# Kernel tuning notes

Hardware: AMD Instinct MI355X
Metric: run time of the kernel (lower is better)

## Reference

```python
import jax, jax.numpy as jnp
import numpy as np

N, D = 262144, 64
L, K = 4, 1024


def setup_inputs() -> dict:
    key = jax.random.key(0)
    k1, k2 = jax.random.split(key)
    features = jax.random.normal(k1, (N, D), dtype=jnp.float32)
    codebooks = jax.random.normal(k2, (L, K, D), dtype=jnp.float32)
    return {"features": features, "codebooks": codebooks}


def reference(features, codebooks):
    """Residual VQ: per level, nearest-center (L2) argmin, gather, subtract.

    Uses squared distances (same argmin as torch.cdist p=2).
    """

    def step(residuals, centers):
        # ||r - c||^2 = ||r||^2 - 2 r.c + ||c||^2   -> [N, K]
        d = (
            jnp.sum(residuals * residuals, axis=1, keepdims=True)
            - 2.0 * (residuals @ centers.T)
            + jnp.sum(centers * centers, axis=1)
        )
        idx = jnp.argmin(d, axis=1)          # [N] int32
        quantized = centers[idx]             # [N, D] gather
        return residuals - quantized, (quantized, idx)

    _, (quantized_levels, indices) = jax.lax.scan(step, features, codebooks)
    quantized_result = jnp.sum(quantized_levels, axis=0)  # sum over L levels
    return quantized_result, indices  # indices: [L, N]
```

## Files before the change

### kernel.cpp

```cpp
#include <hip/hip_runtime.h>
#include <math.h>

constexpr int RVQ_N = 262144;
constexpr int RVQ_D = 64;
constexpr int RVQ_L = 4;
constexpr int RVQ_K = 1024;

typedef __attribute__((ext_vector_type(8))) short short8;
typedef __attribute__((ext_vector_type(4))) float floatx4;

__device__ __forceinline__ unsigned short f2bf(float f) {
  unsigned int u = __float_as_uint(f);
  u += 0x7fffu + ((u >> 16) & 1u);
  return (unsigned short)(u >> 16);
}
__device__ __forceinline__ float bf2f(unsigned short h) {
  return __uint_as_float(((unsigned int)h) << 16);
}
__device__ __forceinline__ void split2(float x, unsigned short& h0,
                                       unsigned short& h1) {
  h0 = f2bf(x);
  float r1 = x - bf2f(h0);
  h1 = f2bf(r1);
}

__global__ __launch_bounds__(256) void rvq_prep_split(
    const float* __restrict__ cb, unsigned short* __restrict__ bh,
    unsigned short* __restrict__ bm) {
  int i = blockIdx.x * 256 + threadIdx.x;
  float c2 = -2.0f * cb[i];
  unsigned short h0, h1;
  split2(c2, h0, h1);
  bh[i] = h0;
  bm[i] = h1;
}

__global__ __launch_bounds__(256) void rvq_cnorm_kernel(
    const float* __restrict__ cb, float* __restrict__ cnorm) {
  int i = blockIdx.x * blockDim.x + threadIdx.x;
  const float* c = cb + (size_t)i * RVQ_D;
  float a0 = 0.f, a1 = 0.f, a2 = 0.f, a3 = 0.f;
#pragma unroll
  for (int d = 0; d < RVQ_D; d += 4) {
    float4 v = *reinterpret_cast<const float4*>(c + d);
    a0 = fmaf(v.x, v.x, a0);
    a1 = fmaf(v.y, v.y, a1);
    a2 = fmaf(v.z, v.z, a2);
    a3 = fmaf(v.w, v.w, a3);
  }
  cnorm[i] = (a0 + a1) + (a2 + a3);
}

__device__ __forceinline__ int raddr(int wbase, int p, int d) {
  return d * 256 + wbase + ((p + d) & 63);
}

__device__ __forceinline__ void merge16(float& a1, int& ai1, float& a2,
                                        int& ai2) {
#pragma unroll
  for (int off = 1; off <= 8; off <<= 1) {
    float ob1 = __shfl_xor(a1, off);
    int oi1 = __shfl_xor(ai1, off);
    float ob2 = __shfl_xor(a2, off);
    int oi2 = __shfl_xor(ai2, off);
    bool aw = (a1 < ob1) || (a1 == ob1 && ai1 <= oi1);
    float w1 = aw ? a1 : ob1;
    int wi1 = aw ? ai1 : oi1;
    float l1 = aw ? ob1 : a1;
    int li1 = aw ? oi1 : ai1;
    float w2 = aw ? a2 : ob2;
    int wi2 = aw ? ai2 : oi2;
    bool sw = (l1 < w2) || (l1 == w2 && li1 < wi2);
    a1 = w1;
    ai1 = wi1;
    a2 = sw ? l1 : w2;
    ai2 = sw ? li1 : wi2;
  }
}

__device__ __forceinline__ void load_bt(const unsigned short* __restrict__ bh,
                                        const unsigned short* __restrict__ bmp,
                                        const float* __restrict__ cnl, int nt,
                                        int m, int q, short8 (&b)[2][2],
                                        float& cc) {
  size_t rowoff = (size_t)(nt * 16 + m) * RVQ_D + q * 8;
  b[0][0] = *(const short8*)(bh + rowoff);
  b[0][1] = *(const short8*)(bh + rowoff + 32);
  b[1][0] = *(const short8*)(bmp + rowoff);
  b[1][1] = *(const short8*)(bmp + rowoff + 32);
  cc = cnl[nt * 16 + m];
}

__global__ __launch_bounds__(256, 2) void rvq_mfma_kernel(
    const float* __restrict__ feat, const float* __restrict__ cb,
    const unsigned short* __restrict__ cb_hi,
    const unsigned short* __restrict__ cb_mid,
    const float* __restrict__ cnorm, float* __restrict__ out_q,
    float* __restrict__ out_idx) {
  __shared__ float rlds[RVQ_D * 256];

  const int tid = threadIdx.x;
  const int lane = tid & 63;
  const int wave = tid >> 6;
  const int wbase = wave * 64;
  const int m = lane & 15;
  const int q = lane >> 4;
  const int g = blockIdx.x * 256 + tid;

  {
    const float4* f4 = (const float4*)(feat + (size_t)g * RVQ_D);
#pragma unroll
    for (int i = 0; i < 16; ++i) {
      float4 v = f4[i];
      rlds[raddr(wbase, lane, 4 * i + 0)] = v.x;
      rlds[raddr(wbase, lane, 4 * i + 1)] = v.y;
      rlds[raddr(wbase, lane, 4 * i + 2)] = v.z;
      rlds[raddr(wbase, lane, 4 * i + 3)] = v.w;
    }
  }
  __syncthreads();

  constexpr int AC[3] = {0, 0, 1};
  constexpr int BC[3] = {0, 1, 0};

  for (int l = 0; l < RVQ_L; ++l) {
    const unsigned short* bh = cb_hi + (size_t)l * RVQ_K * RVQ_D;
    const unsigned short* bmp = cb_mid + (size_t)l * RVQ_K * RVQ_D;
    const float* cnl = cnorm + (size_t)l * RVQ_K;
    const float* cbl = cb + (size_t)l * RVQ_K * RVQ_D;

    short8 afr[4][2][2];
#pragma unroll
    for (int t = 0; t < 4; ++t)
#pragma unroll
      for (int oct = 0; oct < 2; ++oct)
#pragma unroll
        for (int j = 0; j < 8; ++j) {
          int d = oct * 32 + q * 8 + j;
          float x = rlds[raddr(wbase, t * 16 + m, d)];
          unsigned short h0, h1;
          split2(x, h0, h1);
          afr[t][0][oct][j] = (short)h0;
          afr[t][1][oct][j] = (short)h1;
        }

    float m1[4][4], m2v[4][4];
    int i1[4][4], i2v[4][4];
#pragma unroll
    for (int t = 0; t < 4; ++t)
#pragma unroll
      for (int r2 = 0; r2 < 4; ++r2) {
        m1[t][r2] = INFINITY;
        m2v[t][r2] = INFINITY;
        i1[t][r2] = 0;
        i2v[t][r2] = 0;
      }

    short8 bA[2][2], bB[2][2];
    float ccA, ccB;
    load_bt(bh, bmp, cnl, 0, m, q, bA, ccA);

    for (int nt = 0; nt < RVQ_K / 16; nt += 2) {
      load_bt(bh, bmp, cnl, nt + 1, m, q, bB, ccB);

      {
        floatx4 acc[4];
#pragma unroll
        for (int t = 0; t < 4; ++t) {
          acc[t][0] = ccA;
          acc[t][1] = ccA;
          acc[t][2] = ccA;
          acc[t][3] = ccA;
        }
#pragma unroll
        for (int s = 0; s < 3; ++s)
#pragma unroll
          for (int oct = 0; oct < 2; ++oct)
#pragma unroll
            for (int t = 0; t < 4; ++t)
              acc[t] = __builtin_amdgcn_mfma_f32_16x16x32_bf16(
                  afr[t][AC[s]][oct], bA[BC[s]][oct], acc[t], 0, 0, 0);
        int kidx = nt * 16 + m;
#pragma unroll
        for (int t = 0; t < 4; ++t)
#pragma unroll
          for (int r2 = 0; r2 < 4; ++r2) {
            float sc = acc[t][r2];
            float om1 = m1[t][r2];
            bool b1 = sc < om1;
            bool b2 = sc < m2v[t][r2];
            m1[t][r2] = fminf(sc, om1);
            m2v[t][r2] = fminf(fmaxf(sc, om1), m2v[t][r2]);
            i2v[t][r2] = b1 ? i1[t][r2] : (b2 ? kidx : i2v[t][r2]);
            i1[t][r2] = b1 ? kidx : i1[t][r2];
          }
      }

      int ntn = (nt + 2 < RVQ_K / 16) ? nt + 2 : nt;
      load_bt(bh, bmp, cnl, ntn, m, q, bA, ccA);

      {
        floatx4 acc[4];
#pragma unroll
        for (int t = 0; t < 4; ++t) {
          acc[t][0] = ccB;
          acc[t][1] = ccB;
          acc[t][2] = ccB;
          acc[t][3] = ccB;
        }
#pragma unroll
        for (int s = 0; s < 3; ++s)
#pragma unroll
          for (int oct = 0; oct < 2; ++oct)
#pragma unroll
            for (int t = 0; t < 4; ++t)
              acc[t] = __builtin_amdgcn_mfma_f32_16x16x32_bf16(
                  afr[t][AC[s]][oct], bB[BC[s]][oct], acc[t], 0, 0, 0);
        int kidx = (nt + 1) * 16 + m;
#pragma unroll
        for (int t = 0; t < 4; ++t)
#pragma unroll
          for (int r2 = 0; r2 < 4; ++r2) {
            float sc = acc[t][r2];
            float om1 = m1[t][r2];
            bool b1 = sc < om1;
            bool b2 = sc < m2v[t][r2];
            m1[t][r2] = fminf(sc, om1);
            m2v[t][r2] = fminf(fmaxf(sc, om1), m2v[t][r2]);
            i2v[t][r2] = b1 ? i1[t][r2] : (b2 ? kidx : i2v[t][r2]);
            i1[t][r2] = b1 ? kidx : i1[t][r2];
          }
      }
    }

    int cand[4] = {0, 0, 0, 0};
    const int srcl = ((lane >> 2) & 3) << 4;
#pragma unroll
    for (int t = 0; t < 4; ++t)
#pragma unroll
      for (int r2 = 0; r2 < 4; ++r2) {
        float p1 = m1[t][r2], p2 = m2v[t][r2];
        int gi1 = i1[t][r2], gi2 = i2v[t][r2];
        merge16(p1, gi1, p2, gi2);
        float x1 = m1[t][r2], x2 = m2v[t][r2];
        int y1 = i1[t][r2], y2 = i2v[t][r2];
        if (y1 == gi1 || y1 == gi2) x1 = INFINITY;
        if (y2 == gi1 || y2 == gi2) x2 = INFINITY;
        if (x2 < x1 || (x2 == x1 && y2 < y1)) {
          float tf = x1; x1 = x2; x2 = tf;
          int ti = y1; y1 = y2; y2 = ti;
        }
        merge16(x1, y1, x2, y2);
        int v1 = __shfl(gi1, srcl);
        int v2 = __shfl(gi2, srcl);
        int v3 = __shfl(y1, srcl);
        int v4 = __shfl(y2, srcl);
        bool take = (q == t) && ((lane & 3) == r2);
        cand[0] = take ? v1 : cand[0];
        cand[1] = take ? v2 : cand[1];
        cand[2] = take ? v3 : cand[2];
        cand[3] = take ? v4 : cand[3];
      }

    {
      int tmp;
      if (cand[0] > cand[1]) { tmp = cand[0]; cand[0] = cand[1]; cand[1] = tmp; }
      if (cand[2] > cand[3]) { tmp = cand[2]; cand[2] = cand[3]; cand[3] = tmp; }
      if (cand[0] > cand[2]) { tmp = cand[0]; cand[0] = cand[2]; cand[2] = tmp; }
      if (cand[1] > cand[3]) { tmp = cand[1]; cand[1] = cand[3]; cand[3] = tmp; }
      if (cand[1] > cand[2]) { tmp = cand[1]; cand[1] = cand[2]; cand[2] = tmp; }
    }

    float r_[RVQ_D];
#pragma unroll
    for (int d = 0; d < RVQ_D; ++d) r_[d] = rlds[raddr(wbase, lane, d)];

    float s0 = 0.f, s1 = 0.f, s2 = 0.f, s3 = 0.f;
#pragma unroll
    for (int i = 0; i < 16; ++i) {
      s0 = fmaf(r_[4 * i + 0], r_[4 * i + 0], s0);
      s1 = fmaf(r_[4 * i + 1], r_[4 * i + 1], s1);
      s2 = fmaf(r_[4 * i + 2], r_[4 * i + 2], s2);
      s3 = fmaf(r_[4 * i + 3], r_[4 * i + 3], s3);
    }
    const float rr = (s0 + s1) + (s2 + s3);

    float best = INFINITY;
    int ci = 0;
#pragma unroll
    for (int jc = 0; jc < 4; ++jc) {
      int k = cand[jc];
      const float4* c4 = (const float4*)(cbl + (size_t)k * RVQ_D);
      float a0 = 0.f, a1 = 0.f, a2 = 0.f, a3 = 0.f;
#pragma unroll
      for (int i = 0; i < 16; ++i) {
        float4 v = c4[i];
        a0 = fmaf(r_[4 * i + 0], v.x, a0);
        a1 = fmaf(r_[4 * i + 1], v.y, a1);
        a2 = fmaf(r_[4 * i + 2], v.z, a2);
        a3 = fmaf(r_[4 * i + 3], v.w, a3);
      }
      float dot = (a0 + a1) + (a2 + a3);
      float score = (rr - 2.0f * dot) + cnl[k];
      if (score < best) {
        best = score;
        ci = k;
      }
    }

    const float4* crow = (const float4*)(cbl + (size_t)ci * RVQ_D);
    if (l < RVQ_L - 1) {
#pragma unroll
      for (int i = 0; i < 16; ++i) {
        float4 v = crow[i];
        rlds[raddr(wbase, lane, 4 * i + 0)] = r_[4 * i + 0] - v.x;
        rlds[raddr(wbase, lane, 4 * i + 1)] = r_[4 * i + 1] - v.y;
        rlds[raddr(wbase, lane, 4 * i + 2)] = r_[4 * i + 2] - v.z;
        rlds[raddr(wbase, lane, 4 * i + 3)] = r_[4 * i + 3] - v.w;
      }
    } else {
      const float4* f4 = (const float4*)(feat + (size_t)g * RVQ_D);
      float4* o4 = (float4*)(out_q + (size_t)g * RVQ_D);
#pragma unroll
      for (int i = 0; i < 16; ++i) {
        float4 v = crow[i];
        float4 f = f4[i];
        float rn0 = r_[4 * i + 0] - v.x;
        float rn1 = r_[4 * i + 1] - v.y;
        float rn2 = r_[4 * i + 2] - v.z;
        float rn3 = r_[4 * i + 3] - v.w;
        float4 o;
        o.x = f.x - rn0;
        o.y = f.y - rn1;
        o.z = f.z - rn2;
        o.w = f.w - rn3;
        o4[i] = o;
      }
    }
    out_idx[(size_t)l * RVQ_N + g] = (float)ci;
    __syncthreads();
  }
}

extern "C" void kernel_launch(void* const* d_in, const int* in_sizes, int n_in,
                              void* d_out, int out_size, void* d_ws,
                              size_t ws_size, hipStream_t stream) {
  const float* features = (const float*)d_in[0];
  const float* codebooks = (const float*)d_in[1];
  float* out_q = (float*)d_out;
  float* out_idx = (float*)d_out + (size_t)RVQ_N * RVQ_D;

  const size_t comp_elems = (size_t)RVQ_L * RVQ_K * RVQ_D;
  unsigned short* cb_hi = (unsigned short*)d_ws;
  unsigned short* cb_mid = cb_hi + comp_elems;
  float* cnorm = (float*)(cb_mid + comp_elems);

  hipLaunchKernelGGL(rvq_prep_split, dim3(comp_elems / 256), dim3(256), 0,
                     stream, codebooks, cb_hi, cb_mid);
  hipLaunchKernelGGL(rvq_cnorm_kernel, dim3((RVQ_L * RVQ_K) / 256), dim3(256),
                     0, stream, codebooks, cnorm);
  hipLaunchKernelGGL(rvq_mfma_kernel, dim3(RVQ_N / 256), dim3(256), 0, stream,
                     features, codebooks, cb_hi, cb_mid, cnorm, out_q,
                     out_idx);
}
```

Before: 1.102 ms.

## Pack score and tile index into sortable uint keys, drop LDS residual buffer

Distance scores are offset by a constant (cnorm+256) so they stay positive, then their low mantissa bits are replaced by the tile index. Top-2 tracking becomes plain unsigned min/max, and the cross-lane merge becomes four shuffle-min passes. The shared-memory residual buffer and its block barriers are removed: residuals are rebuilt each level from features minus the previously chosen codewords, read from global memory, and occupancy is raised to 3 blocks. The risks are extra global/cache traffic for rebuilding residuals, and loss of score precision in the truncated bits, which the exact fp32 rescoring of 4 candidates must absorb.

```diff
diff --git a/kernel.cpp b/kernel.cpp
--- a/kernel.cpp
+++ b/kernel.cpp
@@ -22,6 +22,12 @@
   h0 = f2bf(x);
   float r1 = x - bf2f(h0);
   h1 = f2bf(r1);
+}
+__device__ __forceinline__ void load8(const float* p, float* v) {
+  float4 a = *(const float4*)p;
+  float4 b = *(const float4*)(p + 4);
+  v[0] = a.x; v[1] = a.y; v[2] = a.z; v[3] = a.w;
+  v[4] = b.x; v[5] = b.y; v[6] = b.z; v[7] = b.w;
 }
 
 __global__ __launch_bounds__(256) void rvq_prep_split(
@@ -36,7 +42,8 @@
 }
 
 __global__ __launch_bounds__(256) void rvq_cnorm_kernel(
-    const float* __restrict__ cb, float* __restrict__ cnorm) {
+    const float* __restrict__ cb, float* __restrict__ cnorm,
+    float* __restrict__ cnormB) {
   int i = blockIdx.x * blockDim.x + threadIdx.x;
   const float* c = cb + (size_t)i * RVQ_D;
   float a0 = 0.f, a1 = 0.f, a2 = 0.f, a3 = 0.f;
@@ -48,34 +55,9 @@
     a2 = fmaf(v.z, v.z, a2);
     a3 = fmaf(v.w, v.w, a3);
   }
-  cnorm[i] = (a0 + a1) + (a2 + a3);
-}
-
-__device__ __forceinline__ int raddr(int wbase, int p, int d) {
-  return d * 256 + wbase + ((p + d) & 63);
-}
-
-__device__ __forceinline__ void merge16(float& a1, int& ai1, float& a2,
-                                        int& ai2) {
-#pragma unroll
-  for (int off = 1; off <= 8; off <<= 1) {
-    float ob1 = __shfl_xor(a1, off);
-    int oi1 = __shfl_xor(ai1, off);
-    float ob2 = __shfl_xor(a2, off);
-    int oi2 = __shfl_xor(ai2, off);
-    bool aw = (a1 < ob1) || (a1 == ob1 && ai1 <= oi1);
-    float w1 = aw ? a1 : ob1;
-    int wi1 = aw ? ai1 : oi1;
-    float l1 = aw ? ob1 : a1;
-    int li1 = aw ? oi1 : ai1;
-    float w2 = aw ? a2 : ob2;
-    int wi2 = aw ? ai2 : oi2;
-    bool sw = (l1 < w2) || (l1 == w2 && li1 < wi2);
-    a1 = w1;
-    ai1 = wi1;
-    a2 = sw ? l1 : w2;
-    ai2 = sw ? li1 : wi2;
-  }
+  float s = (a0 + a1) + (a2 + a3);
+  cnorm[i] = s;
+  cnormB[i] = s + 256.0f;
 }
 
 __device__ __forceinline__ void load_bt(const unsigned short* __restrict__ bh,
@@ -91,86 +73,98 @@
   cc = cnl[nt * 16 + m];
 }
 
-__global__ __launch_bounds__(256, 2) void rvq_mfma_kernel(
+__global__ __launch_bounds__(256, 3) void rvq_mfma_kernel(
     const float* __restrict__ feat, const float* __restrict__ cb,
     const unsigned short* __restrict__ cb_hi,
     const unsigned short* __restrict__ cb_mid,
-    const float* __restrict__ cnorm, float* __restrict__ out_q,
-    float* __restrict__ out_idx) {
-  __shared__ float rlds[RVQ_D * 256];
-
+    const float* __restrict__ cnorm, const float* __restrict__ cnormB,
+    float* __restrict__ out_q, float* __restrict__ out_idx) {
   const int tid = threadIdx.x;
   const int lane = tid & 63;
   const int wave = tid >> 6;
-  const int wbase = wave * 64;
   const int m = lane & 15;
   const int q = lane >> 4;
-  const int g = blockIdx.x * 256 + tid;
-
-  {
-    const float4* f4 = (const float4*)(feat + (size_t)g * RVQ_D);
-#pragma unroll
-    for (int i = 0; i < 16; ++i) {
-      float4 v = f4[i];
-      rlds[raddr(wbase, lane, 4 * i + 0)] = v.x;
-      rlds[raddr(wbase, lane, 4 * i + 1)] = v.y;
-      rlds[raddr(wbase, lane, 4 * i + 2)] = v.z;
-      rlds[raddr(wbase, lane, 4 * i + 3)] = v.w;
-    }
-  }
-  __syncthreads();
+  const int base = blockIdx.x * 256 + wave * 64;
+  const int g = base + lane;
+
+  int ci0 = 0, ci1 = 0, ci2 = 0;
 
   constexpr int AC[3] = {0, 0, 1};
   constexpr int BC[3] = {0, 1, 0};
 
+#pragma unroll
   for (int l = 0; l < RVQ_L; ++l) {
     const unsigned short* bh = cb_hi + (size_t)l * RVQ_K * RVQ_D;
     const unsigned short* bmp = cb_mid + (size_t)l * RVQ_K * RVQ_D;
+    const float* cnBl = cnormB + (size_t)l * RVQ_K;
     const float* cnl = cnorm + (size_t)l * RVQ_K;
     const float* cbl = cb + (size_t)l * RVQ_K * RVQ_D;
 
     short8 afr[4][2][2];
 #pragma unroll
+    for (int t = 0; t < 4; ++t) {
+      const int p = t * 16 + m;
+      int j0 = 0, j1 = 0, j2 = 0;
+      if (l > 0) j0 = __shfl(ci0, p);
+      if (l > 1) j1 = __shfl(ci1, p);
+      if (l > 2) j2 = __shfl(ci2, p);
+      const float* fp = feat + (size_t)(base + p) * RVQ_D;
+      const float* c0p = cb + (size_t)j0 * RVQ_D;
+      const float* c1p = cb + ((size_t)RVQ_K + j1) * RVQ_D;
+      const float* c2p = cb + ((size_t)2 * RVQ_K + j2) * RVQ_D;
+#pragma unroll
+      for (int oct = 0; oct < 2; ++oct) {
+        const int dof = oct * 32 + q * 8;
+        float v[8];
+        load8(fp + dof, v);
+        if (l > 0) {
+          float c[8];
+          load8(c0p + dof, c);
+#pragma unroll
+          for (int e = 0; e < 8; ++e) v[e] -= c[e];
+        }
+        if (l > 1) {
+          float c[8];
+          load8(c1p + dof, c);
+#pragma unroll
+          for (int e = 0; e < 8; ++e) v[e] -= c[e];
+        }
+        if (l > 2) {
+          float c[8];
+          load8(c2p + dof, c);
+#pragma unroll
+          for (int e = 0; e < 8; ++e) v[e] -= c[e];
+        }
+#pragma unroll
+        for (int e = 0; e < 8; ++e) {
+          unsigned short h0, h1;
+          split2(v[e], h0, h1);
+          afr[t][0][oct][e] = (short)h0;
+          afr[t][1][oct][e] = (short)h1;
+        }
+      }
+    }
+
+    unsigned p1[4][4], p2[4][4];
+#pragma unroll
     for (int t = 0; t < 4; ++t)
 #pragma unroll
-      for (int oct = 0; oct < 2; ++oct)
-#pragma unroll
-        for (int j = 0; j < 8; ++j) {
-          int d = oct * 32 + q * 8 + j;
-          float x = rlds[raddr(wbase, t * 16 + m, d)];
-          unsigned short h0, h1;
-          split2(x, h0, h1);
-          afr[t][0][oct][j] = (short)h0;
-          afr[t][1][oct][j] = (short)h1;
-        }
-
-    float m1[4][4], m2v[4][4];
-    int i1[4][4], i2v[4][4];
-#pragma unroll
-    for (int t = 0; t < 4; ++t)
-#pragma unroll
       for (int r2 = 0; r2 < 4; ++r2) {
-        m1[t][r2] = INFINITY;
-        m2v[t][r2] = INFINITY;
-        i1[t][r2] = 0;
-        i2v[t][r2] = 0;
+        p1[t][r2] = 0xFFFFFFFFu;
+        p2[t][r2] = 0xFFFFFFFFu;
       }
 
     short8 bA[2][2], bB[2][2];
     float ccA, ccB;
-    load_bt(bh, bmp, cnl, 0, m, q, bA, ccA);
+    load_bt(bh, bmp, cnBl, 0, m, q, bA, ccA);
 
     for (int nt = 0; nt < RVQ_K / 16; nt += 2) {
-      load_bt(bh, bmp, cnl, nt + 1, m, q, bB, ccB);
-
+      load_bt(bh, bmp, cnBl, nt + 1, m, q, bB, ccB);
       {
         floatx4 acc[4];
 #pragma unroll
         for (int t = 0; t < 4; ++t) {
-          acc[t][0] = ccA;
-          acc[t][1] = ccA;
-          acc[t][2] = ccA;
-          acc[t][3] = ccA;
+          acc[t][0] = ccA; acc[t][1] = ccA; acc[t][2] = ccA; acc[t][3] = ccA;
         }
 #pragma unroll
         for (int s = 0; s < 3; ++s)
@@ -180,33 +174,24 @@
             for (int t = 0; t < 4; ++t)
               acc[t] = __builtin_amdgcn_mfma_f32_16x16x32_bf16(
                   afr[t][AC[s]][oct], bA[BC[s]][oct], acc[t], 0, 0, 0);
-        int kidx = nt * 16 + m;
+        unsigned nbits = (unsigned)nt;
 #pragma unroll
         for (int t = 0; t < 4; ++t)
 #pragma unroll
           for (int r2 = 0; r2 < 4; ++r2) {
-            float sc = acc[t][r2];
-            float om1 = m1[t][r2];
-            bool b1 = sc < om1;
-            bool b2 = sc < m2v[t][r2];
-            m1[t][r2] = fminf(sc, om1);
-            m2v[t][r2] = fminf(fmaxf(sc, om1), m2v[t][r2]);
-            i2v[t][r2] = b1 ? i1[t][r2] : (b2 ? kidx : i2v[t][r2]);
-            i1[t][r2] = b1 ? kidx : i1[t][r2];
+            unsigned u = (__float_as_uint(acc[t][r2]) & 0xFFFFFFC0u) | nbits;
+            unsigned mx = p1[t][r2] > u ? p1[t][r2] : u;
+            p1[t][r2] = p1[t][r2] < u ? p1[t][r2] : u;
+            p2[t][r2] = p2[t][r2] < mx ? p2[t][r2] : mx;
           }
       }
-
       int ntn = (nt + 2 < RVQ_K / 16) ? nt + 2 : nt;
-      load_bt(bh, bmp, cnl, ntn, m, q, bA, ccA);
-
+      load_bt(bh, bmp, cnBl, ntn, m, q, bA, ccA);
       {
         floatx4 acc[4];
 #pragma unroll
         for (int t = 0; t < 4; ++t) {
-          acc[t][0] = ccB;
-          acc[t][1] = ccB;
-          acc[t][2] = ccB;
-          acc[t][3] = ccB;
+          acc[t][0] = ccB; acc[t][1] = ccB; acc[t][2] = ccB; acc[t][3] = ccB;
         }
 #pragma unroll
         for (int s = 0; s < 3; ++s)
@@ -216,19 +201,15 @@
             for (int t = 0; t < 4; ++t)
               acc[t] = __builtin_amdgcn_mfma_f32_16x16x32_bf16(
                   afr[t][AC[s]][oct], bB[BC[s]][oct], acc[t], 0, 0, 0);
-        int kidx = (nt + 1) * 16 + m;
+        unsigned nbits = (unsigned)(nt + 1);
 #pragma unroll
         for (int t = 0; t < 4; ++t)
 #pragma unroll
           for (int r2 = 0; r2 < 4; ++r2) {
-            float sc = acc[t][r2];
-            float om1 = m1[t][r2];
-            bool b1 = sc < om1;
-            bool b2 = sc < m2v[t][r2];
-            m1[t][r2] = fminf(sc, om1);
-            m2v[t][r2] = fminf(fmaxf(sc, om1), m2v[t][r2]);
-            i2v[t][r2] = b1 ? i1[t][r2] : (b2 ? kidx : i2v[t][r2]);
-            i1[t][r2] = b1 ? kidx : i1[t][r2];
+            unsigned u = (__float_as_uint(acc[t][r2]) & 0xFFFFFFC0u) | nbits;
+            unsigned mx = p1[t][r2] > u ? p1[t][r2] : u;
+            p1[t][r2] = p1[t][r2] < u ? p1[t][r2] : u;
+            p2[t][r2] = p2[t][r2] < mx ? p2[t][r2] : mx;
           }
       }
     }
@@ -239,27 +220,32 @@
     for (int t = 0; t < 4; ++t)
 #pragma unroll
       for (int r2 = 0; r2 < 4; ++r2) {
-        float p1 = m1[t][r2], p2 = m2v[t][r2];
-        int gi1 = i1[t][r2], gi2 = i2v[t][r2];
-        merge16(p1, gi1, p2, gi2);
-        float x1 = m1[t][r2], x2 = m2v[t][r2];
-        int y1 = i1[t][r2], y2 = i2v[t][r2];
-        if (y1 == gi1 || y1 == gi2) x1 = INFINITY;
-        if (y2 == gi1 || y2 == gi2) x2 = INFINITY;
-        if (x2 < x1 || (x2 == x1 && y2 < y1)) {
-          float tf = x1; x1 = x2; x2 = tf;
-          int ti = y1; y1 = y2; y2 = ti;
-        }
-        merge16(x1, y1, x2, y2);
-        int v1 = __shfl(gi1, srcl);
-        int v2 = __shfl(gi2, srcl);
-        int v3 = __shfl(y1, srcl);
-        int v4 = __shfl(y2, srcl);
+        unsigned a = p1[t][r2], b = p2[t][r2];
+        int ka = (int)((a & 63u) << 4) | m;
+        int kb = (int)((b & 63u) << 4) | m;
+        unsigned va = (a & 0xFFFFFC00u) | (unsigned)ka;
+        unsigned vb = (b & 0xFFFFFC00u) | (unsigned)kb;
+        if (vb < va) { unsigned tu = va; va = vb; vb = tu; }
+        int ck[4];
+#pragma unroll
+        for (int pass = 0; pass < 4; ++pass) {
+          unsigned gm = va;
+#pragma unroll
+          for (int off = 1; off <= 8; off <<= 1) {
+            unsigned o = (unsigned)__shfl_xor((int)gm, off);
+            gm = gm < o ? gm : o;
+          }
+          ck[pass] = (int)(gm & 1023u);
+          bool hit = (va == gm);
+          va = hit ? vb : va;
+          vb = hit ? 0xFFFFFFFFu : vb;
+        }
+        int v1 = __shfl(ck[0], srcl);
+        int v2 = __shfl(ck[1], srcl);
+        int v3 = __shfl(ck[2], srcl);
+        int v4 = __shfl(ck[3], srcl);
         bool take = (q == t) && ((lane & 3) == r2);
-        cand[0] = take ? v1 : cand[0];
-        cand[1] = take ? v2 : cand[1];
-        cand[2] = take ? v3 : cand[2];
-        cand[3] = take ? v4 : cand[3];
+        if (take) { cand[0] = v1; cand[1] = v2; cand[2] = v3; cand[3] = v4; }
       }
 
     {
@@ -272,8 +258,43 @@
     }
 
     float r_[RVQ_D];
-#pragma unroll
-    for (int d = 0; d < RVQ_D; ++d) r_[d] = rlds[raddr(wbase, lane, d)];
+    {
+      const float4* f4p = (const float4*)(feat + (size_t)g * RVQ_D);
+#pragma unroll
+      for (int i = 0; i < 16; ++i) {
+        float4 v = f4p[i];
+        r_[4 * i + 0] = v.x; r_[4 * i + 1] = v.y;
+        r_[4 * i + 2] = v.z; r_[4 * i + 3] = v.w;
+      }
+      if (l > 0) {
+        const float4* cp = (const float4*)(cb + (size_t)ci0 * RVQ_D);
+#pragma unroll
+        for (int i = 0; i < 16; ++i) {
+          float4 v = cp[i];
+          r_[4 * i + 0] -= v.x; r_[4 * i + 1] -= v.y;
+          r_[4 * i + 2] -= v.z; r_[4 * i + 3] -= v.w;
+        }
+      }
+      if (l > 1) {
+        const float4* cp = (const float4*)(cb + ((size_t)RVQ_K + ci1) * RVQ_D);
+#pragma unroll
+        for (int i = 0; i < 16; ++i) {
+          float4 v = cp[i];
+          r_[4 * i + 0] -= v.x; r_[4 * i + 1] -= v.y;
+          r_[4 * i + 2] -= v.z; r_[4 * i + 3] -= v.w;
+        }
+      }
+      if (l > 2) {
+        const float4* cp =
+            (const float4*)(cb + ((size_t)2 * RVQ_K + ci2) * RVQ_D);
+#pragma unroll
+        for (int i = 0; i < 16; ++i) {
+          float4 v = cp[i];
+          r_[4 * i + 0] -= v.x; r_[4 * i + 1] -= v.y;
+          r_[4 * i + 2] -= v.z; r_[4 * i + 3] -= v.w;
+        }
+      }
+    }
 
     float s0 = 0.f, s1 = 0.f, s2 = 0.f, s3 = 0.f;
 #pragma unroll
@@ -308,37 +329,31 @@
       }
     }
 
-    const float4* crow = (const float4*)(cbl + (size_t)ci * RVQ_D);
-    if (l < RVQ_L - 1) {
+    if (l == 0) ci0 = ci;
+    else if (l == 1) ci1 = ci;
+    else if (l == 2) ci2 = ci;
+
+    if (l == RVQ_L - 1) {
+      const float4* crow = (const float4*)(cbl + (size_t)ci * RVQ_D);
+      const float4* f4p = (const float4*)(feat + (size_t)g * RVQ_D);
+      float4* o4 = (float4*)(out_q + (size_t)g * RVQ_D);
 #pragma unroll
       for (int i = 0; i < 16; ++i) {
-        float4 v = crow[i];
-        rlds[raddr(wbase, lane, 4 * i + 0)] = r_[4 * i + 0] - v.x;
-        rlds[raddr(wbase, lane, 4 * i + 1)] = r_[4 * i + 1] - v.y;
-        rlds[raddr(wbase, lane, 4 * i + 2)] = r_[4 * i + 2] - v.z;
-        rlds[raddr(wbase, lane, 4 * i + 3)] = r_[4 * i + 3] - v.w;
-      }
-    } else {
-      const float4* f4 = (const float4*)(feat + (size_t)g * RVQ_D);
-      float4* o4 = (float4*)(out_q + (size_t)g * RVQ_D);
-#pragma unroll
-      for (int i = 0; i < 16; ++i) {
-        float4 v = crow[i];
-        float4 f = f4[i];
-        float rn0 = r_[4 * i + 0] - v.x;
-        float rn1 = r_[4 * i + 1] - v.y;
-        float rn2 = r_[4 * i + 2] - v.z;
-        float rn3 = r_[4 * i + 3] - v.w;
+        float4 cv = crow[i];
+        float4 fv = f4p[i];
+        float rn0 = r_[4 * i + 0] - cv.x;
+        float rn1 = r_[4 * i + 1] - cv.y;
+        float rn2 = r_[4 * i + 2] - cv.z;
+        float rn3 = r_[4 * i + 3] - cv.w;
         float4 o;
-        o.x = f.x - rn0;
-        o.y = f.y - rn1;
-        o.z = f.z - rn2;
-        o.w = f.w - rn3;
+        o.x = fv.x - rn0;
+        o.y = fv.y - rn1;
+        o.z = fv.z - rn2;
+        o.w = fv.w - rn3;
         o4[i] = o;
       }
     }
     out_idx[(size_t)l * RVQ_N + g] = (float)ci;
-    __syncthreads();
   }
 }
 
@@ -354,12 +369,13 @@
   unsigned short* cb_hi = (unsigned short*)d_ws;
   unsigned short* cb_mid = cb_hi + comp_elems;
   float* cnorm = (float*)(cb_mid + comp_elems);
+  float* cnormB = cnorm + (size_t)RVQ_L * RVQ_K;
 
   hipLaunchKernelGGL(rvq_prep_split, dim3(comp_elems / 256), dim3(256), 0,
                      stream, codebooks, cb_hi, cb_mid);
   hipLaunchKernelGGL(rvq_cnorm_kernel, dim3((RVQ_L * RVQ_K) / 256), dim3(256),
-                     0, stream, codebooks, cnorm);
+                     0, stream, codebooks, cnorm, cnormB);
   hipLaunchKernelGGL(rvq_mfma_kernel, dim3(RVQ_N / 256), dim3(256), 0, stream,
-                     features, codebooks, cb_hi, cb_mid, cnorm, out_q,
+                     features, codebooks, cb_hi, cb_mid, cnorm, cnormB, out_q,
                      out_idx);
 }
```

After: 974.6 us. 11.6% less time.
